# Kernel tuning notes

Measured on AMD Instinct MI355X. Metric: run time of the kernel, lower is better.

## Reference

```python
import jax, jax.numpy as jnp
import numpy as np

N, E, G = 50000, 800000, 128
F_IN, H, NHID, C = 310, 128, 64, 2  # H = 2*nhid
NEG_SLOPE = 0.2


def setup_inputs() -> dict:
    key = jax.random.key(0)
    ks = jax.random.split(key, 16)
    def lin(k, fan_in, shape):
        return (jax.random.normal(k, shape, jnp.float32) / np.sqrt(fan_in)).astype(jnp.float32)
    return {
        "x": jax.random.normal(ks[0], (N, F_IN), jnp.float32),
        "edge_index": jax.random.randint(ks[1], (2, E), 0, N, dtype=jnp.int32),
        "batch": jnp.sort(jax.random.randint(ks[2], (N,), 0, G, dtype=jnp.int32)),
        "W1": lin(ks[3], F_IN, (F_IN, H)),
        "a_src1": lin(ks[4], H, (H,)),
        "a_dst1": lin(ks[5], H, (H,)),
        "b1": jnp.zeros((H,), jnp.float32),
        "W2": lin(ks[6], H, (H, H)),
        "a_src2": lin(ks[7], H, (H,)),
        "a_dst2": lin(ks[8], H, (H,)),
        "b2": jnp.zeros((H,), jnp.float32),
        "fc1_w": lin(ks[9], H, (H, NHID)),
        "fc1_b": jnp.zeros((NHID,), jnp.float32),
        "fc2_w": lin(ks[10], NHID, (NHID, C)),
        "fc2_b": jnp.zeros((C,), jnp.float32),
    }


def _gat(x, src, dst, W, a_src, a_dst, b):
    # PyG GATConv, heads=1: h = xW; e_ij = LeakyReLU(a_src.h_j + a_dst.h_i)
    h = x @ W                               # [N, H]
    asrc = h @ a_src                        # [N]
    adst = h @ a_dst                        # [N]
    e = jax.nn.leaky_relu(asrc[src] + adst[dst], NEG_SLOPE)  # [E']
    # segment softmax over incoming edges of each target node
    m = jax.ops.segment_max(e, dst, num_segments=N)
    ex = jnp.exp(e - m[dst])
    s = jax.ops.segment_sum(ex, dst, num_segments=N)
    w = ex / s[dst]                         # [E']
    out = jax.ops.segment_sum(h[src] * w[:, None], dst, num_segments=N)
    return out + b


def reference(x, edge_index, batch, W1, a_src1, a_dst1, b1,
              W2, a_src2, a_dst2, b2, fc1_w, fc1_b, fc2_w, fc2_b):
    # add self loops (GATConv default add_self_loops=True)
    ar = jnp.arange(N, dtype=edge_index.dtype)
    src = jnp.concatenate([edge_index[0], ar])
    dst = jnp.concatenate([edge_index[1], ar])

    h = jax.nn.selu(_gat(x, src, dst, W1, a_src1, a_dst1, b1))
    h = jax.nn.selu(_gat(h, src, dst, W2, a_src2, a_dst2, b2))

    # global mean pool over graphs
    summed = jax.ops.segment_sum(h, batch, num_segments=G)          # [G, H]
    cnt = jax.ops.segment_sum(jnp.ones((N,), h.dtype), batch, num_segments=G)
    pooled = jax.nn.selu(summed / jnp.maximum(cnt, 1.0)[:, None])

    z = jax.nn.selu(pooled @ fc1_w + fc1_b)  # dropout is identity in eval
    logits = z @ fc2_w + fc2_b
    return jax.nn.log_softmax(logits, axis=-1)
```

## Files before the change

### kernel.cpp

```cpp
#include <hip/hip_runtime.h>
#include <hip/hip_bf16.h>
#include <math.h>

#define NN 50000
#define NE 800000
#define NET (NE + NN)
#define FIN 310
#define HD 128
#define NHID 64
#define NCLS 2
#define NG 128
#define NEG_SLOPE 0.2f
#define KP1 320
#define KP2 128

#define SLOTS 64
#define NPART 8
#define PART_SZ (NN / NPART)
#define EPB 4096
#define NSLICE ((NET + EPB - 1) / EPB)

#define SELU_SCALE 1.0507009873554804934193349852946f
#define SELU_ALPHA 1.6732632423543772848170429916717f

typedef short bf16x8 __attribute__((ext_vector_type(8)));
typedef float f32x4 __attribute__((ext_vector_type(4)));

__device__ __forceinline__ float selu(float x) {
    return SELU_SCALE * (x > 0.f ? x : SELU_ALPHA * (__expf(x) - 1.f));
}
__device__ __forceinline__ float lrelu(float x) {
    return x > 0.f ? x : NEG_SLOPE * x;
}
__device__ __forceinline__ unsigned short f2bf(float f) {
    unsigned int u = __float_as_uint(f);
    u = (u + 0x7fffu + ((u >> 16) & 1u)) >> 16;
    return (unsigned short)u;
}
__device__ __forceinline__ float bf2f(unsigned short b) {
    return __uint_as_float(((unsigned int)b) << 16);
}


__global__ __launch_bounds__(256) void k_scatter_slots(const int* __restrict__ ei,
                                                       int* __restrict__ cursor,
                                                       unsigned short* __restrict__ slots) {
    int part = blockIdx.x / NSLICE;
    int slice = blockIdx.x - part * NSLICE;
    int lo = part * PART_SZ;
    int base = slice * EPB + threadIdx.x;
#pragma unroll
    for (int k = 0; k < EPB / 256; ++k) {
        int i = base + k * 256;
        if (i >= NET) break;
        int d = (i < NE) ? __builtin_nontemporal_load(ei + NE + i) : (i - NE);
        if ((unsigned)(d - lo) < (unsigned)PART_SZ) {
            int s = (i < NE) ? __builtin_nontemporal_load(ei + i) : d;
            int pos = atomicAdd(&cursor[d], 1) & (SLOTS - 1);
            slots[(size_t)d * SLOTS + pos] = (unsigned short)s;
        }
    }
}


__global__ void k_castW(const float* __restrict__ W1, const float* __restrict__ W2,
                        unsigned short* __restrict__ W1p, unsigned short* __restrict__ W2p,
                        int* __restrict__ cursor) {
    int i = blockIdx.x * blockDim.x + threadIdx.x;
    if (i < NN) cursor[i] = 0;
    const int N1 = HD * KP1;
    if (i < N1) {
        int n = i / KP1, k = i % KP1;
        unsigned short v = (k < FIN) ? f2bf(W1[(size_t)k * HD + n]) : (unsigned short)0;
        W1p[((k >> 3) * HD + n) * 8 + (k & 7)] = v;
    } else {
        int j = i - N1;
        if (j < HD * KP2) {
            int n = j / KP2, k = j % KP2;
            W2p[((k >> 3) * HD + n) * 8 + (k & 7)] = f2bf(W2[(size_t)k * HD + n]);
        }
    }
}


#define RGEMM_EPILOGUE                                                         \
    int gr_base = r0 + w * 16 + quad * 4;                                      \
    _Pragma("unroll")                                                          \
    for (int r = 0; r < 4; ++r) {                                              \
        int gr = gr_base + r;                                                  \
        if (gr < M) {                                                          \
            _Pragma("unroll")                                                  \
            for (int nt = 0; nt < 8; ++nt)                                     \
                C[(size_t)gr * HD + nt * 16 + l16] = f2bf(acc[nt][r]);         \
        }                                                                      \
    }                                                                          \
    _Pragma("unroll")                                                          \
    for (int r = 0; r < 4; ++r) {                                              \
        float s1 = 0.f, s2 = 0.f;                                              \
        _Pragma("unroll")                                                      \
        for (int nt = 0; nt < 8; ++nt) {                                       \
            int c = nt * 16 + l16;                                             \
            float v = acc[nt][r];                                              \
            s1 += v * a_src[c];                                                \
            s2 += v * a_dst[c];                                                \
        }                                                                      \
        _Pragma("unroll")                                                      \
        for (int off = 1; off < 16; off <<= 1) {                               \
            s1 += __shfl_xor(s1, off);                                         \
            s2 += __shfl_xor(s2, off);                                         \
        }                                                                      \
        int gr = gr_base + r;                                                  \
        if (l16 == 0 && gr < M) { asrcp[gr] = s1; adstp[gr] = s2; }            \
    }


__global__ __launch_bounds__(256) void k_gemm1(const float* __restrict__ A,
                                               const unsigned short* __restrict__ Bp,
                                               unsigned short* __restrict__ C,
                                               float* __restrict__ asrcp,
                                               float* __restrict__ adstp,
                                               const float* __restrict__ a_src,
                                               const float* __restrict__ a_dst,
                                               int M) {
    int t = threadIdx.x;
    int lane = t & 63, w = t >> 6;
    int quad = lane >> 4, l16 = lane & 15;
    int r0 = blockIdx.x * 64;

    int grow = r0 + w * 16 + l16;
    int arow = min(grow, M - 1);
    const float* aptr = A + (size_t)arow * FIN + quad * 8;

    f32x4 acc[8] = {};
#pragma unroll 2
    for (int k0 = 0; k0 < 288; k0 += 32) {
        const float* ap = aptr + k0;
        float2 f0 = *(const float2*)(ap + 0);
        float2 f1 = *(const float2*)(ap + 2);
        float2 f2 = *(const float2*)(ap + 4);
        float2 f3 = *(const float2*)(ap + 6);
        union { bf16x8 v; unsigned short u[8]; } af;
        af.u[0] = f2bf(f0.x); af.u[1] = f2bf(f0.y);
        af.u[2] = f2bf(f1.x); af.u[3] = f2bf(f1.y);
        af.u[4] = f2bf(f2.x); af.u[5] = f2bf(f2.y);
        af.u[6] = f2bf(f3.x); af.u[7] = f2bf(f3.y);
        const unsigned short* bbase = Bp + ((size_t)(k0 >> 3) + quad) * (HD * 8) + l16 * 8;
#pragma unroll
        for (int nt = 0; nt < 8; ++nt) {
            bf16x8 bfr = *(const bf16x8*)(bbase + nt * 128);
            acc[nt] = __builtin_amdgcn_mfma_f32_16x16x32_bf16(af.v, bfr, acc[nt], 0, 0, 0);
        }
    }
    {
        int kb = 288 + quad * 8;
        union { bf16x8 v; unsigned short u[8]; } af;
#pragma unroll
        for (int j = 0; j < 8; ++j)
            af.u[j] = (kb + j < FIN) ? f2bf(aptr[288 + j]) : (unsigned short)0;
        const unsigned short* bbase = Bp + ((size_t)(288 >> 3) + quad) * (HD * 8) + l16 * 8;
#pragma unroll
        for (int nt = 0; nt < 8; ++nt) {
            bf16x8 bfr = *(const bf16x8*)(bbase + nt * 128);
            acc[nt] = __builtin_amdgcn_mfma_f32_16x16x32_bf16(af.v, bfr, acc[nt], 0, 0, 0);
        }
    }
    RGEMM_EPILOGUE
}


__global__ __launch_bounds__(256) void k_gemm2(const unsigned short* __restrict__ A,
                                               const unsigned short* __restrict__ Bp,
                                               unsigned short* __restrict__ C,
                                               float* __restrict__ asrcp,
                                               float* __restrict__ adstp,
                                               const float* __restrict__ a_src,
                                               const float* __restrict__ a_dst,
                                               int M) {
    int t = threadIdx.x;
    int lane = t & 63, w = t >> 6;
    int quad = lane >> 4, l16 = lane & 15;
    int r0 = blockIdx.x * 64;

    int grow = r0 + w * 16 + l16;
    int arow = min(grow, M - 1);
    const unsigned short* aptr = A + (size_t)arow * KP2 + quad * 8;

    f32x4 acc[8] = {};
#pragma unroll
    for (int k0 = 0; k0 < KP2; k0 += 32) {
        bf16x8 af = *(const bf16x8*)(aptr + k0);
        const unsigned short* bbase = Bp + ((size_t)(k0 >> 3) + quad) * (HD * 8) + l16 * 8;
#pragma unroll
        for (int nt = 0; nt < 8; ++nt) {
            bf16x8 bfr = *(const bf16x8*)(bbase + nt * 128);
            acc[nt] = __builtin_amdgcn_mfma_f32_16x16x32_bf16(af, bfr, acc[nt], 0, 0, 0);
        }
    }
    RGEMM_EPILOGUE
}


__global__ __launch_bounds__(256) void k_gat(const unsigned short* __restrict__ h,
                                             const float* __restrict__ asrc,
                                             const float* __restrict__ adst,
                                             const int* __restrict__ degv,
                                             const unsigned short* __restrict__ slots,
                                             const float* __restrict__ bias,
                                             unsigned short* __restrict__ out) {
    int node = blockIdx.x * 4 + (threadIdx.x >> 6);
    int lane = threadIdx.x & 63;
    if (node >= NN) return;
    int g = lane >> 4, cl = lane & 15;
    int deg = degv[node];
    float adsti = adst[node];

    float2 acc2[4] = {};

    int cnt = min(deg, SLOTS);
    int s_c = 0; float p_c = 0.f;
    if (lane < cnt) {
        s_c = slots[(size_t)node * SLOTS + lane];
        p_c = __expf(lrelu(asrc[s_c] + adsti));
    }
    float den_l = p_c;
    int nt = (cnt + 3) >> 2;
    for (int t = 0; t < nt; t += 2) {
        float pv[2]; uint4 hv[2];
#pragma unroll
        for (int u = 0; u < 2; ++u) {
            int tt = t + u;
            bool valid = tt < nt;
            int e = (4 * tt + g) & 63;
            int s = __shfl(s_c, e);
            float p = __shfl(p_c, e);
            int sa = valid ? s : 0;
            pv[u] = valid ? p : 0.f;
            hv[u] = *(const uint4*)(h + (size_t)sa * HD + cl * 8);
        }
#pragma unroll
        for (int u = 0; u < 2; ++u) {
            float p = pv[u];
            unsigned int w0 = hv[u].x, w1 = hv[u].y, w2 = hv[u].z, w3 = hv[u].w;
            acc2[0].x += p * __uint_as_float(w0 << 16);
            acc2[0].y += p * __uint_as_float(w0 & 0xffff0000u);
            acc2[1].x += p * __uint_as_float(w1 << 16);
            acc2[1].y += p * __uint_as_float(w1 & 0xffff0000u);
            acc2[2].x += p * __uint_as_float(w2 << 16);
            acc2[2].y += p * __uint_as_float(w2 & 0xffff0000u);
            acc2[3].x += p * __uint_as_float(w3 << 16);
            acc2[3].y += p * __uint_as_float(w3 & 0xffff0000u);
        }
    }
#pragma unroll
    for (int k = 0; k < 4; ++k) {
        acc2[k].x += __shfl_xor(acc2[k].x, 16);
        acc2[k].y += __shfl_xor(acc2[k].y, 16);
        acc2[k].x += __shfl_xor(acc2[k].x, 32);
        acc2[k].y += __shfl_xor(acc2[k].y, 32);
    }
#pragma unroll
    for (int off = 32; off; off >>= 1)
        den_l += __shfl_xor(den_l, off);

    if (g == 0) {
        float inv = 1.f / den_l;
        int c0 = cl * 8;
        float4 b0 = *(const float4*)(bias + c0);
        float4 b1 = *(const float4*)(bias + c0 + 4);
        float v0 = selu(acc2[0].x * inv + b0.x);
        float v1 = selu(acc2[0].y * inv + b0.y);
        float v2 = selu(acc2[1].x * inv + b0.z);
        float v3 = selu(acc2[1].y * inv + b0.w);
        float v4 = selu(acc2[2].x * inv + b1.x);
        float v5 = selu(acc2[2].y * inv + b1.y);
        float v6 = selu(acc2[3].x * inv + b1.z);
        float v7 = selu(acc2[3].y * inv + b1.w);
        uint4 pk;
        pk.x = (unsigned int)f2bf(v0) | ((unsigned int)f2bf(v1) << 16);
        pk.y = (unsigned int)f2bf(v2) | ((unsigned int)f2bf(v3) << 16);
        pk.z = (unsigned int)f2bf(v4) | ((unsigned int)f2bf(v5) << 16);
        pk.w = (unsigned int)f2bf(v6) | ((unsigned int)f2bf(v7) << 16);
        *(uint4*)(out + (size_t)node * HD + c0) = pk;
    }
}


__device__ __forceinline__ int lower_bound_i(const int* a, int n, int key) {
    int lo = 0, hi = n;
    while (lo < hi) {
        int mid = (lo + hi) >> 1;
        if (a[mid] < key) lo = mid + 1; else hi = mid;
    }
    return lo;
}

__global__ __launch_bounds__(512) void k_poolfc(const unsigned short* __restrict__ x,
                                                const int* __restrict__ batch,
                                                const float* __restrict__ w1,
                                                const float* __restrict__ b1,
                                                const float* __restrict__ w2,
                                                const float* __restrict__ b2,
                                                float* __restrict__ out) {
    int g = blockIdx.x;
    int t = threadIdx.x;
    __shared__ int lo_s, hi_s;
    __shared__ float red[512];
    __shared__ float pooled_s[128];
    if (t == 0) {
        lo_s = lower_bound_i(batch, NN, g);
        hi_s = lower_bound_i(batch, NN, g + 1);
    }
    __syncthreads();
    int lo = lo_s, hi = hi_s;
    float acc = 0.f;
    for (int n = lo + (t >> 7); n < hi; n += 4)
        acc += bf2f(x[(size_t)n * HD + (t & 127)]);
    red[t] = acc;
    __syncthreads();
    if (t < 128) {
        float v = red[t] + red[t + 128] + red[t + 256] + red[t + 384];
        pooled_s[t] = selu(v / fmaxf((float)(hi - lo), 1.f));
    }
    __syncthreads();
    if (t < 64) {
        float z = 0.f;
#pragma unroll 8
        for (int k = 0; k < HD; ++k) z += pooled_s[k] * w1[k * NHID + t];
        z = selu(z + b1[t]);
        float p0 = z * w2[t * NCLS + 0];
        float p1 = z * w2[t * NCLS + 1];
        for (int off = 32; off; off >>= 1) {
            p0 += __shfl_down(p0, off);
            p1 += __shfl_down(p1, off);
        }
        if (t == 0) {
            float l0 = p0 + b2[0], l1 = p1 + b2[1];
            float m = fmaxf(l0, l1);
            float lse = m + __logf(__expf(l0 - m) + __expf(l1 - m));
            out[g * NCLS + 0] = l0 - lse;
            out[g * NCLS + 1] = l1 - lse;
        }
    }
}


static inline size_t align_up(size_t v, size_t a) { return (v + a - 1) / a * a; }

extern "C" void kernel_launch(void* const* d_in, const int* in_sizes, int n_in,
                              void* d_out, int out_size, void* d_ws, size_t ws_size,
                              hipStream_t stream) {
    const float* x      = (const float*)d_in[0];
    const int*   ei     = (const int*)d_in[1];
    const int*   batch  = (const int*)d_in[2];
    const float* W1     = (const float*)d_in[3];
    const float* a_src1 = (const float*)d_in[4];
    const float* a_dst1 = (const float*)d_in[5];
    const float* b1     = (const float*)d_in[6];
    const float* W2     = (const float*)d_in[7];
    const float* a_src2 = (const float*)d_in[8];
    const float* a_dst2 = (const float*)d_in[9];
    const float* b2     = (const float*)d_in[10];
    const float* fc1_w  = (const float*)d_in[11];
    const float* fc1_b  = (const float*)d_in[12];
    const float* fc2_w  = (const float*)d_in[13];
    const float* fc2_b  = (const float*)d_in[14];
    float* out = (float*)d_out;

    char* ws = (char*)d_ws;
    size_t off = 0;
    unsigned short* h1  = (unsigned short*)(ws + off); off = align_up(off + (size_t)NN * HD * 2, 256);
    unsigned short* o1  = (unsigned short*)(ws + off); off = align_up(off + (size_t)NN * HD * 2, 256);
    float* asrc = (float*)(ws + off); off = align_up(off + (size_t)NN * 4, 256);
    float* adst = (float*)(ws + off); off = align_up(off + (size_t)NN * 4, 256);
    int* cursor = (int*)(ws + off);   off = align_up(off + (size_t)NN * 4, 256);
    unsigned short* slots = (unsigned short*)(ws + off); off = align_up(off + (size_t)NN * SLOTS * 2, 256);
    unsigned short* W1p = (unsigned short*)(ws + off); off = align_up(off + (size_t)HD * KP1 * 2, 256);
    unsigned short* W2p = (unsigned short*)(ws + off); off = align_up(off + (size_t)HD * KP2 * 2, 256);
    (void)ws_size;

    k_castW<<<(HD * (KP1 + KP2) + 255) / 256, 256, 0, stream>>>(W1, W2, W1p, W2p, cursor);

    k_scatter_slots<<<NPART * NSLICE, 256, 0, stream>>>(ei, cursor, slots);

    int gblocks = (NN + 63) / 64;

    k_gemm1<<<gblocks, 256, 0, stream>>>(x, W1p, h1, asrc, adst, a_src1, a_dst1, NN);
    k_gat<<<(NN + 3) / 4, 256, 0, stream>>>(h1, asrc, adst, cursor, slots, b1, o1);

    k_gemm2<<<gblocks, 256, 0, stream>>>(o1, W2p, h1, asrc, adst, a_src2, a_dst2, NN);
    k_gat<<<(NN + 3) / 4, 256, 0, stream>>>(h1, asrc, adst, cursor, slots, b2, o1);

    k_poolfc<<<NG, 512, 0, stream>>>(o1, batch, fc1_w, fc1_b, fc2_w, fc2_b, out);
}
```

Before: 304.9 us.

## Pre-pack x to bf16 tiled layout, stage weights in LDS, interleave scatter partitions

Adds a separate kernel that converts x to bf16 in an MFMA-fragment-friendly tiled layout, so gemm1 reads contiguous packed A fragments instead of strided fp32 rows it converts itself. Both GEMMs now copy the whole packed weight matrix into shared memory before the MFMA loop. The slot-scatter kernel interleaves partitions across adjacent blocks and drops nontemporal loads so edge data can be reused from cache. The cost is an extra pass writing and rereading a 32MB bf16 copy of x, plus 80KB of LDS per gemm1 block, which limits occupancy.

```diff
diff --git a/kernel.cpp b/kernel.cpp
--- a/kernel.cpp
+++ b/kernel.cpp
@@ -12,6 +12,7 @@
 #define NG 128
 #define NEG_SLOPE 0.2f
 #define KP1 320
+#define PKB1 (KP1 / 8)
 #define KP2 128
 
 #define SLOTS 64
@@ -45,21 +46,47 @@
 __global__ __launch_bounds__(256) void k_scatter_slots(const int* __restrict__ ei,
                                                        int* __restrict__ cursor,
                                                        unsigned short* __restrict__ slots) {
-    int part = blockIdx.x / NSLICE;
-    int slice = blockIdx.x - part * NSLICE;
+    int part = blockIdx.x & (NPART - 1);
+    int slice = blockIdx.x >> 3;
     int lo = part * PART_SZ;
     int base = slice * EPB + threadIdx.x;
 #pragma unroll
     for (int k = 0; k < EPB / 256; ++k) {
         int i = base + k * 256;
         if (i >= NET) break;
-        int d = (i < NE) ? __builtin_nontemporal_load(ei + NE + i) : (i - NE);
+        int d = (i < NE) ? ei[NE + i] : (i - NE);
         if ((unsigned)(d - lo) < (unsigned)PART_SZ) {
-            int s = (i < NE) ? __builtin_nontemporal_load(ei + i) : d;
+            int s = (i < NE) ? ei[i] : d;
             int pos = atomicAdd(&cursor[d], 1) & (SLOTS - 1);
             slots[(size_t)d * SLOTS + pos] = (unsigned short)s;
         }
     }
+}
+
+
+__global__ __launch_bounds__(256) void k_castx(const float* __restrict__ x,
+                                               unsigned short* __restrict__ Ap) {
+    int i = blockIdx.x * blockDim.x + threadIdx.x;
+    if (i >= NN * PKB1) return;
+    int row = i / PKB1, kb = i - row * PKB1;
+    int k = kb * 8;
+    union { bf16x8 v; unsigned short u[8]; uint4 q; } af;
+    const float* src = x + (size_t)row * FIN + k;
+    if (k + 8 <= FIN) {
+        float2 f0 = *(const float2*)(src);
+        float2 f1 = *(const float2*)(src + 2);
+        float2 f2 = *(const float2*)(src + 4);
+        float2 f3 = *(const float2*)(src + 6);
+        af.u[0] = f2bf(f0.x); af.u[1] = f2bf(f0.y);
+        af.u[2] = f2bf(f1.x); af.u[3] = f2bf(f1.y);
+        af.u[4] = f2bf(f2.x); af.u[5] = f2bf(f2.y);
+        af.u[6] = f2bf(f3.x); af.u[7] = f2bf(f3.y);
+    } else {
+#pragma unroll
+        for (int j = 0; j < 8; ++j)
+            af.u[j] = (k + j < FIN) ? f2bf(src[j]) : (unsigned short)0;
+    }
+    *(uint4*)(Ap + ((((size_t)(row >> 4)) * PKB1 + kb) * 16 + (row & 15)) * 8) = af.q;
 }
 
 
@@ -114,7 +141,7 @@
     }
 
 
-__global__ __launch_bounds__(256) void k_gemm1(const float* __restrict__ A,
+__global__ __launch_bounds__(256) void k_gemm1(const unsigned short* __restrict__ Ap,
                                                const unsigned short* __restrict__ Bp,
                                                unsigned short* __restrict__ C,
                                                float* __restrict__ asrcp,
@@ -122,46 +149,27 @@
                                                const float* __restrict__ a_src,
                                                const float* __restrict__ a_dst,
                                                int M) {
+    __shared__ unsigned short Bs[KP1 * HD];
     int t = threadIdx.x;
     int lane = t & 63, w = t >> 6;
     int quad = lane >> 4, l16 = lane & 15;
     int r0 = blockIdx.x * 64;
 
-    int grow = r0 + w * 16 + l16;
-    int arow = min(grow, M - 1);
-    const float* aptr = A + (size_t)arow * FIN + quad * 8;
+    for (int j = t; j < KP1 * HD / 8; j += 256)
+        ((uint4*)Bs)[j] = ((const uint4*)Bp)[j];
+    __syncthreads();
+
+    const unsigned short* apack = Ap + (((size_t)(blockIdx.x * 4 + w) * PKB1) * 16 + l16) * 8;
 
     f32x4 acc[8] = {};
-#pragma unroll 2
-    for (int k0 = 0; k0 < 288; k0 += 32) {
-        const float* ap = aptr + k0;
-        float2 f0 = *(const float2*)(ap + 0);
-        float2 f1 = *(const float2*)(ap + 2);
-        float2 f2 = *(const float2*)(ap + 4);
-        float2 f3 = *(const float2*)(ap + 6);
-        union { bf16x8 v; unsigned short u[8]; } af;
-        af.u[0] = f2bf(f0.x); af.u[1] = f2bf(f0.y);
-        af.u[2] = f2bf(f1.x); af.u[3] = f2bf(f1.y);
-        af.u[4] = f2bf(f2.x); af.u[5] = f2bf(f2.y);
-        af.u[6] = f2bf(f3.x); af.u[7] = f2bf(f3.y);
-        const unsigned short* bbase = Bp + ((size_t)(k0 >> 3) + quad) * (HD * 8) + l16 * 8;
+#pragma unroll
+    for (int k0 = 0; k0 < KP1; k0 += 32) {
+        bf16x8 af = *(const bf16x8*)(apack + (size_t)((k0 >> 3) + quad) * 128);
+        const unsigned short* bbase = Bs + ((k0 >> 3) + quad) * (HD * 8) + l16 * 8;
 #pragma unroll
         for (int nt = 0; nt < 8; ++nt) {
             bf16x8 bfr = *(const bf16x8*)(bbase + nt * 128);
-            acc[nt] = __builtin_amdgcn_mfma_f32_16x16x32_bf16(af.v, bfr, acc[nt], 0, 0, 0);
-        }
-    }
-    {
-        int kb = 288 + quad * 8;
-        union { bf16x8 v; unsigned short u[8]; } af;
-#pragma unroll
-        for (int j = 0; j < 8; ++j)
-            af.u[j] = (kb + j < FIN) ? f2bf(aptr[288 + j]) : (unsigned short)0;
-        const unsigned short* bbase = Bp + ((size_t)(288 >> 3) + quad) * (HD * 8) + l16 * 8;
-#pragma unroll
-        for (int nt = 0; nt < 8; ++nt) {
-            bf16x8 bfr = *(const bf16x8*)(bbase + nt * 128);
-            acc[nt] = __builtin_amdgcn_mfma_f32_16x16x32_bf16(af.v, bfr, acc[nt], 0, 0, 0);
+            acc[nt] = __builtin_amdgcn_mfma_f32_16x16x32_bf16(af, bfr, acc[nt], 0, 0, 0);
         }
     }
     RGEMM_EPILOGUE
@@ -176,11 +184,16 @@
                                                const float* __restrict__ a_src,
                                                const float* __restrict__ a_dst,
                                                int M) {
+    __shared__ unsigned short Bs[KP2 * HD];
     int t = threadIdx.x;
     int lane = t & 63, w = t >> 6;
     int quad = lane >> 4, l16 = lane & 15;
     int r0 = blockIdx.x * 64;
 
+    for (int j = t; j < KP2 * HD / 8; j += 256)
+        ((uint4*)Bs)[j] = ((const uint4*)Bp)[j];
+    __syncthreads();
+
     int grow = r0 + w * 16 + l16;
     int arow = min(grow, M - 1);
     const unsigned short* aptr = A + (size_t)arow * KP2 + quad * 8;
@@ -189,7 +202,7 @@
 #pragma unroll
     for (int k0 = 0; k0 < KP2; k0 += 32) {
         bf16x8 af = *(const bf16x8*)(aptr + k0);
-        const unsigned short* bbase = Bp + ((size_t)(k0 >> 3) + quad) * (HD * 8) + l16 * 8;
+        const unsigned short* bbase = Bs + ((k0 >> 3) + quad) * (HD * 8) + l16 * 8;
 #pragma unroll
         for (int nt = 0; nt < 8; ++nt) {
             bf16x8 bfr = *(const bf16x8*)(bbase + nt * 128);
@@ -368,6 +381,7 @@
 
     char* ws = (char*)d_ws;
     size_t off = 0;
+    unsigned short* Apack = (unsigned short*)(ws + off); off = align_up(off + (size_t)NN * KP1 * 2, 256);
     unsigned short* h1  = (unsigned short*)(ws + off); off = align_up(off + (size_t)NN * HD * 2, 256);
     unsigned short* o1  = (unsigned short*)(ws + off); off = align_up(off + (size_t)NN * HD * 2, 256);
     float* asrc = (float*)(ws + off); off = align_up(off + (size_t)NN * 4, 256);
@@ -380,11 +394,13 @@
 
     k_castW<<<(HD * (KP1 + KP2) + 255) / 256, 256, 0, stream>>>(W1, W2, W1p, W2p, cursor);
 
-    k_scatter_slots<<<NPART * NSLICE, 256, 0, stream>>>(ei, cursor, slots);
+    k_castx<<<(NN * PKB1 + 255) / 256, 256, 0, stream>>>(x, Apack);
+
+    k_scatter_slots<<<NSLICE * NPART, 256, 0, stream>>>(ei, cursor, slots);
 
     int gblocks = (NN + 63) / 64;
 
-    k_gemm1<<<gblocks, 256, 0, stream>>>(x, W1p, h1, asrc, adst, a_src1, a_dst1, NN);
+    k_gemm1<<<gblocks, 256, 0, stream>>>(Apack, W1p, h1, asrc, adst, a_src1, a_dst1, NN);
     k_gat<<<(NN + 3) / 4, 256, 0, stream>>>(h1, asrc, adst, cursor, slots, b1, o1);
 
     k_gemm2<<<gblocks, 256, 0, stream>>>(o1, W2p, h1, asrc, adst, a_src2, a_dst2, NN);
```

After: 325.5 us. 6.7% more time.
